# Performance work log

Measured on AMD Instinct MI355X. Metric: run time of the kernel, lower is better.

Reference implementation:

```python
import jax, jax.numpy as jnp
import numpy as np

IN_FEATURES = 512
OUT_FEATURES = 1024
BATCH = 1024
LAMBD = 0.2
TOL = 1e-4
MAX_ITERS = 100


def setup_inputs() -> dict:
    key = jax.random.key(0)
    kx, kw = jax.random.split(key)
    x = jax.random.normal(kx, (BATCH, IN_FEATURES), dtype=jnp.float32)
    # weight ~ randn(out, in), normalized over dim=0 (per-column) as in torch
    w = jax.random.normal(kw, (OUT_FEATURES, IN_FEATURES), dtype=jnp.float32)
    w = w / jnp.linalg.norm(w, axis=0)
    # M_inv = inverse(A^T A + I)^T with A = weight.T of shape (N, M)
    A = w.T  # (N, M)
    Mmat = A.T @ A + jnp.eye(OUT_FEATURES, dtype=jnp.float32)  # (M, M)
    M_inv = jnp.linalg.inv(Mmat).T
    return {"x": x, "weight": w, "M_inv": M_inv}


def _softshrink(x, lambd):
    return jnp.sign(x) * jnp.maximum(jnp.abs(x) - lambd, 0.0)


def _admm(A_dot_b, M_inv, lambd):
    # Fixed-length scan with per-sample freeze masks, equivalent to the
    # torch loop that removes converged rows from the active batch.
    B, M = A_dot_b.shape
    z = jnp.zeros((B, M), A_dot_b.dtype)
    solved0 = jnp.zeros((B,), dtype=bool)
    # carry: (v, u, v_prev, v_solution, solved)
    def step(carry, _):
        v, u, v_prev, v_sol, solved = carry
        b_eff = A_dot_b + v - u               # (B, M)
        xk = b_eff @ M_inv                    # (B, M)
        v_new = _softshrink(xk + u, lambd)
        u_new = u + xk - v_new
        dx_norm = jnp.linalg.norm(v_new - v_prev, axis=1)
        x_norm = jnp.linalg.norm(v_new, axis=1)
        conv = (dx_norm / x_norm) < TOL       # nan (0/0) compares False, as torch
        newly = conv & (~solved)
        v_sol = jnp.where(newly[:, None], v_new, v_sol)
        solved = solved | newly
        active = ~solved
        # frozen (solved) rows stop updating, mirroring removal from the batch
        v2 = jnp.where(active[:, None], v_new, v)
        u2 = jnp.where(active[:, None], u_new, u)
        return (v2, u2, v2, v_sol, solved), None

    carry0 = (z, z, z, z, solved0)
    (v, u, v_prev, v_sol, solved), _ = jax.lax.scan(step, carry0, None, length=MAX_ITERS)
    # torch returns v_solution (zeros for never-converged samples)
    return v_sol


def reference(x, weight, M_inv):
    input_shape = x.shape
    b = jax.lax.stop_gradient(x.reshape(x.shape[0], -1))  # x.detach().flatten(1)
    A_dot_b = b @ weight.T  # b @ A with A = weight.T -> (B, M)
    encoded = _admm(A_dot_b, M_inv, LAMBD)  # (B, M)
    decoded = encoded @ weight              # (B, N)
    return encoded, decoded.reshape(input_shape)
```

## Files before the change

### kernel.cpp

```cpp
#include <hip/hip_runtime.h>

typedef _Float16 half8 __attribute__((ext_vector_type(8)));
typedef _Float16 half4 __attribute__((ext_vector_type(4)));
typedef float floatx4 __attribute__((ext_vector_type(4)));
typedef float floatx16 __attribute__((ext_vector_type(16)));

static constexpr int BATCH = 1024;
static constexpr int NIN   = 512;
static constexpr int MOUT  = 1024;
static constexpr float LAMBD = 0.2f;
static constexpr float TOLF  = 1e-4f;
static constexpr int MAX_ITERS = 100;
static constexpr int MM = BATCH * MOUT;

__device__ __forceinline__ size_t swz(int idx, int k) {
    return ((((size_t)(idx >> 4) * 32 + (k >> 5)) * 64 +
             ((idx & 15) | (((k >> 3) & 3) << 4))) << 3) + (k & 7);
}

__device__ __forceinline__ size_t swz32(int idx, int k) {
    return ((((size_t)(idx >> 5) * 64 + (k >> 4)) * 64 +
             ((idx & 31) | (((k >> 3) & 1) << 5))) << 3) + (k & 7);
}

__device__ __forceinline__ float shrinkf(float t) {
    float a = fabsf(t) - LAMBD;
    return a > 0.f ? copysignf(a, t) : 0.f;
}

__device__ __forceinline__ void gbar32(int* cnt, int* gen, int seq) {
    __syncthreads();
    if (threadIdx.x == 0) {
        int old = atomicAdd(cnt, 1);
        if (old == seq * 32 - 1) {
            __hip_atomic_store(gen, seq, __ATOMIC_RELAXED,
                               __HIP_MEMORY_SCOPE_AGENT);
        } else {
            while (__hip_atomic_load(gen, __ATOMIC_RELAXED,
                                     __HIP_MEMORY_SCOPE_AGENT) < seq)
                __builtin_amdgcn_s_sleep(1);
        }
    }
    __syncthreads();
    asm volatile("buffer_inv sc0" ::: "memory");
}

__global__ __launch_bounds__(256) void zero_init(float* t, float* enc,
                                                 float* dec, float* ench_f,
                                                 float* encl_f, int* solved) {
    int i = blockIdx.x * 256 + threadIdx.x;
    if (i < MM) { t[i] = 0.f; enc[i] = 0.f; }
    if (i < MM / 2) { dec[i] = 0.f; ench_f[i] = 0.f; encl_f[i] = 0.f; }
    if (i < 4096) solved[i] = 0;
}

__global__ __launch_bounds__(256) void split_minv(const float* __restrict__ Minv,
                                                  _Float16* __restrict__ Th,
                                                  _Float16* __restrict__ Tl) {
    int g = blockIdx.x * 256 + threadIdx.x;
    int n = g & 1023, k0 = (g >> 10) << 3;
    half8 h, l;
    #pragma unroll
    for (int e = 0; e < 8; ++e) {
        float val = Minv[(size_t)(k0 + e) * MOUT + n];
        _Float16 hh = (_Float16)val;
        h[e] = hh;
        l[e] = (_Float16)(val - (float)hh);
    }
    size_t off = swz32(n, k0);
    *(half8*)&Th[off] = h;
    *(half8*)&Tl[off] = l;
}

__global__ __launch_bounds__(256) void split_w(const float* __restrict__ w,
                                               _Float16* __restrict__ wsh,
                                               _Float16* __restrict__ wsl) {
    int g = blockIdx.x * 256 + threadIdx.x;
    int n = g & 511, k0 = (g >> 9) << 3;
    half8 h, l;
    #pragma unroll
    for (int e = 0; e < 8; ++e) {
        float val = w[(size_t)(k0 + e) * NIN + n];
        _Float16 hh = (_Float16)val;
        h[e] = hh;
        l[e] = (_Float16)(val - (float)hh);
    }
    size_t off = swz(n, k0);
    *(half8*)&wsh[off] = h;
    *(half8*)&wsl[off] = l;
}

__global__ __launch_bounds__(256) void gemm_adb(const float* __restrict__ x,
                                                const float* __restrict__ w,
                                                float* __restrict__ adb,
                                                _Float16* __restrict__ bh,
                                                _Float16* __restrict__ bl) {
    __shared__ float As[16][68];
    __shared__ float Bs[16][68];
    const int tid = threadIdx.x;
    const int i0 = (blockIdx.x >> 4) * 64, j0 = (blockIdx.x & 15) * 64;
    const int tx = tid & 15, ty = tid >> 4;
    const int lr = tid >> 2, lk = (tid & 3) << 2;
    float acc[4][4] = {};
    for (int k0 = 0; k0 < NIN; k0 += 16) {
        float4 a4 = *(const float4*)&x[(i0 + lr) * NIN + k0 + lk];
        As[lk + 0][lr] = a4.x; As[lk + 1][lr] = a4.y;
        As[lk + 2][lr] = a4.z; As[lk + 3][lr] = a4.w;
        float4 b4 = *(const float4*)&w[(j0 + lr) * NIN + k0 + lk];
        Bs[lk + 0][lr] = b4.x; Bs[lk + 1][lr] = b4.y;
        Bs[lk + 2][lr] = b4.z; Bs[lk + 3][lr] = b4.w;
        __syncthreads();
        #pragma unroll
        for (int kk = 0; kk < 16; ++kk) {
            float4 a_ = *(const float4*)&As[kk][ty << 2];
            float4 b_ = *(const float4*)&Bs[kk][tx << 2];
            #pragma unroll
            for (int r = 0; r < 4; ++r) {
                float av = r == 0 ? a_.x : r == 1 ? a_.y : r == 2 ? a_.z : a_.w;
                acc[r][0] = fmaf(av, b_.x, acc[r][0]);
                acc[r][1] = fmaf(av, b_.y, acc[r][1]);
                acc[r][2] = fmaf(av, b_.z, acc[r][2]);
                acc[r][3] = fmaf(av, b_.w, acc[r][3]);
            }
        }
        __syncthreads();
    }
    const int k4 = j0 + (tx << 2);
    #pragma unroll
    for (int r = 0; r < 4; ++r) {
        const int row = i0 + (ty << 2) + r;
        *(float4*)&adb[(size_t)row * MOUT + k4] =
            make_float4(acc[r][0], acc[r][1], acc[r][2], acc[r][3]);
        half4 h, l;
        #pragma unroll
        for (int e = 0; e < 4; ++e) {
            _Float16 hh = (_Float16)acc[r][e];
            h[e] = hh;
            l[e] = (_Float16)(acc[r][e] - (float)hh);
        }
        size_t off = swz32(row, k4);
        *(half4*)&bh[off] = h;
        *(half4*)&bl[off] = l;
    }
}

__global__ __launch_bounds__(512, 2)
void admm_loop(const float* __restrict__ adb, float* __restrict__ part,
               _Float16* __restrict__ bh0, _Float16* __restrict__ bl0,
               _Float16* __restrict__ bh1, _Float16* __restrict__ bl1,
               const _Float16* __restrict__ Th, const _Float16* __restrict__ Tl,
               float* __restrict__ enc, _Float16* __restrict__ ench,
               _Float16* __restrict__ encl, int* __restrict__ solved,
               int* __restrict__ bar) {
    const int bid = blockIdx.x;
    const int tid = threadIdx.x, lane = tid & 63;
    const int w = tid >> 6;
    const int bt = w >> 1;
    const int kh = w & 1;
    const int mt = bid & 7, nt = bid >> 3;
    const int n0 = nt << 5, m0 = mt << 7;
    const int hn = lane >> 5;
    const int brow = m0 + (bt << 5) + (lane & 31);
    const int btile = (mt << 2) + bt;

    __shared__ _Float16 Bs[128 * 512];
    __shared__ float sc[4][64][24];
    __shared__ int s_exit;

    #pragma unroll
    for (int q = 0; q < 16; ++q) {
        const int chunk = (w << 4) + q;
        const int kc = chunk >> 1, hl = chunk & 1;
        const _Float16* src = (hl ? Tl : Th) +
            (((size_t)((nt << 6) + kc)) << 9) + ((size_t)lane << 3);
        __builtin_amdgcn_global_load_lds(
            (const __attribute__((address_space(1))) void*)src,
            (__attribute__((address_space(3))) void*)&Bs[(size_t)chunk << 9],
            16, 0, 0);
    }
    __syncthreads();

    int* gcnt = bar + (mt << 5);
    int* ggen = bar + (mt << 5) + 16;

    float treg[16] = {};
    float adbreg[16];
    #pragma unroll
    for (int r4 = 0; r4 < 4; ++r4) {
        const int nb = n0 + (r4 << 3) + (hn << 2);
        float4 a4 = *(const float4*)&adb[(size_t)brow * MOUT + nb];
        adbreg[(r4 << 2) + 0] = a4.x; adbreg[(r4 << 2) + 1] = a4.y;
        adbreg[(r4 << 2) + 2] = a4.z; adbreg[(r4 << 2) + 3] = a4.w;
    }
    bool sflag = false;

    for (int it = 0; it < MAX_ITERS; ++it) {
        const _Float16* rbh = (it & 1) ? bh1 : bh0;
        const _Float16* rbl = (it & 1) ? bl1 : bl0;
        _Float16* wbh = (it & 1) ? bh0 : bh1;
        _Float16* wbl = (it & 1) ? bl0 : bl1;

        floatx16 accA = {}, accB = {}, accC = {};
        const int kc0 = kh << 5;
        #pragma unroll 4
        for (int kc = kc0; kc < kc0 + 32; ++kc) {
            const size_t boff =
                (((size_t)(btile << 6) + kc) << 9) + ((size_t)lane << 3);
            const half8 bhf = *(const half8*)&rbh[boff];
            const half8 blf = *(const half8*)&rbl[boff];
            const half8 ah = *(const half8*)&Bs[((kc << 1) << 9) + (lane << 3)];
            const half8 al = *(const half8*)&Bs[(((kc << 1) | 1) << 9) + (lane << 3)];
            accA = __builtin_amdgcn_mfma_f32_32x32x16_f16(al, bhf, accA, 0, 0, 0);
            accB = __builtin_amdgcn_mfma_f32_32x32x16_f16(ah, blf, accB, 0, 0, 0);
            accC = __builtin_amdgcn_mfma_f32_32x32x16_f16(ah, bhf, accC, 0, 0, 0);
        }
        if (kh) {
            #pragma unroll
            for (int r4 = 0; r4 < 4; ++r4) {
                float4 v;
                v.x = (accA[(r4 << 2) + 0] + accB[(r4 << 2) + 0]) + accC[(r4 << 2) + 0];
                v.y = (accA[(r4 << 2) + 1] + accB[(r4 << 2) + 1]) + accC[(r4 << 2) + 1];
                v.z = (accA[(r4 << 2) + 2] + accB[(r4 << 2) + 2]) + accC[(r4 << 2) + 2];
                v.w = (accA[(r4 << 2) + 3] + accB[(r4 << 2) + 3]) + accC[(r4 << 2) + 3];
                *(float4*)&sc[bt][lane][r4 << 2] = v;
            }
        }
        __syncthreads();

        float dx2 = 0.f, x2 = 0.f;
        if (kh == 0 && !sflag) {
            #pragma unroll
            for (int r4 = 0; r4 < 4; ++r4) {
                float4 p1 = *(const float4*)&sc[bt][lane][r4 << 2];
                float pa[4] = {p1.x, p1.y, p1.z, p1.w};
                half4 h, l;
                #pragma unroll
                for (int e = 0; e < 4; ++e) {
                    const int r = (r4 << 2) + e;
                    float s0 = (accA[r] + accB[r]) + accC[r];
                    float xk = s0 + pa[e];
                    float t_ = treg[r];
                    float vprev = shrinkf(t_);
                    float uu = t_ - vprev;
                    float tn = xk + uu;
                    float vv = shrinkf(tn);
                    float un = tn - vv;
                    float d = vv - vprev;
                    dx2 += d * d;
                    x2 += vv * vv;
                    treg[r] = tn;
                    float nb_ = (adbreg[r] + vv) - un;
                    _Float16 hh = (_Float16)nb_;
                    h[e] = hh;
                    l[e] = (_Float16)(nb_ - (float)hh);
                }
                size_t off = swz32(brow, n0 + (r4 << 3) + (hn << 2));
                *(half4*)&wbh[off] = h;
                *(half4*)&wbl[off] = l;
            }
            dx2 += __shfl_xor(dx2, 32);
            x2  += __shfl_xor(x2, 32);
            if (hn == 0)
                *(float2*)&part[(((size_t)brow << 5) | nt) << 1] =
                    make_float2(dx2, x2);
        }
        gbar32(gcnt, ggen, 2 * it + 1);

        if (w < 4) {
            const int urow = m0 + (nt << 2) + w;
            if (!((volatile const int*)solved)[urow]) {
                float2 p = *(const float2*)
                    &part[(((size_t)urow << 5) | (lane & 31)) << 1];
                float rdx = p.x, rx = p.y;
                #pragma unroll
                for (int off = 16; off; off >>= 1) {
                    rdx += __shfl_xor(rdx, off);
                    rx  += __shfl_xor(rx, off);
                }
                if (rdx < TOLF * TOLF * rx) {
                    if (lane == 0) ((volatile int*)solved)[urow] = 1;
                }
            }
        }
        gbar32(gcnt, ggen, 2 * it + 2);

        sflag = ((volatile const int*)solved)[brow] != 0;
        if (tid == 0) s_exit = 0;
        __syncthreads();
        if (kh == 0 && !sflag && lane < 32) s_exit = 1;
        __syncthreads();
        if (s_exit == 0) break;
    }

    if (kh == 0 && sflag) {
        #pragma unroll
        for (int r4 = 0; r4 < 4; ++r4) {
            const int nb = n0 + (r4 << 3) + (hn << 2);
            float va[4]; half4 h, l;
            #pragma unroll
            for (int e = 0; e < 4; ++e) {
                float vv = shrinkf(treg[(r4 << 2) + e]);
                va[e] = vv;
                _Float16 hh = (_Float16)vv;
                h[e] = hh;
                l[e] = (_Float16)(vv - (float)hh);
            }
            *(float4*)&enc[(size_t)brow * MOUT + nb] =
                make_float4(va[0], va[1], va[2], va[3]);
            size_t off = swz(brow, nb);
            *(half4*)&ench[off] = h;
            *(half4*)&encl[off] = l;
        }
    }
}

__global__ __launch_bounds__(256, 2)
void mfma_dec(const _Float16* __restrict__ Ahg, const _Float16* __restrict__ Alg,
              const _Float16* __restrict__ Bhg, const _Float16* __restrict__ Blg,
              float* __restrict__ out) {
    constexpr int NSTR = NIN;
    constexpr int NT = NSTR / 128;
    const int bid = blockIdx.x;
    const int c = bid & 7, t = bid >> 3;
    const int mt = t / NT, nt = t % NT;
    const int tid = threadIdx.x, lane = tid & 63;

    __shared__ _Float16 Ash[64 * 512];

    const int wv = tid >> 6;
    const int wm = (tid >> 7) & 1, wn = (tid >> 6) & 1;
    const int kf0 = c << 2;

    #pragma unroll
    for (int i = 0; i < 16; ++i) {
        const int chunk = (wv << 4) + i;
        const int rt = chunk >> 3, kc = (chunk >> 1) & 3, hl = chunk & 1;
        const _Float16* src = (hl ? Alg : Ahg) +
            ((((size_t)((mt << 3) + rt) * 32 + kf0 + kc) << 9) + ((size_t)lane << 3));
        __builtin_amdgcn_global_load_lds(
            (const __attribute__((address_space(1))) void*)src,
            (__attribute__((address_space(3))) void*)&Ash[(size_t)chunk << 9],
            16, 0, 0);
    }
    __syncthreads();

    const int ct0 = nt * 8 + (wn << 2);
    const _Float16* pBh = Bhg + ((((size_t)ct0 * 32 + kf0) * 64 + lane) << 3);
    const _Float16* pBl = Blg + ((((size_t)ct0 * 32 + kf0) * 64 + lane) << 3);

    floatx4 acc[4][4] = {};
    #pragma unroll
    for (int s = 0; s < 4; ++s) {
        half8 bhf[4], blf[4];
        #pragma unroll
        for (int j = 0; j < 4; ++j) {
            bhf[j] = *(const half8*)(pBh + ((size_t)j << 14) + ((size_t)s << 9));
            blf[j] = *(const half8*)(pBl + ((size_t)j << 14) + ((size_t)s << 9));
        }
        half8 ah[4], al[4];
        #pragma unroll
        for (int i = 0; i < 4; ++i) {
            const int rt = (wm << 2) + i;
            ah[i] = *(const half8*)&Ash[((((rt << 2) + s) << 1) << 9) + (lane << 3)];
            al[i] = *(const half8*)&Ash[(((((rt << 2) + s) << 1) + 1) << 9) + (lane << 3)];
        }
        #pragma unroll
        for (int i = 0; i < 4; ++i)
            #pragma unroll
            for (int j = 0; j < 4; ++j) {
                acc[i][j] = __builtin_amdgcn_mfma_f32_16x16x32_f16(
                    ah[i], blf[j], acc[i][j], 0, 0, 0);
                acc[i][j] = __builtin_amdgcn_mfma_f32_16x16x32_f16(
                    al[i], bhf[j], acc[i][j], 0, 0, 0);
                acc[i][j] = __builtin_amdgcn_mfma_f32_16x16x32_f16(
                    ah[i], bhf[j], acc[i][j], 0, 0, 0);
            }
    }

    const int orow = (lane >> 4) << 2;
    #pragma unroll
    for (int i = 0; i < 4; ++i) {
        const int gr = (mt << 7) + (wm << 6) + (i << 4) + orow;
        #pragma unroll
        for (int j = 0; j < 4; ++j) {
            const int gc = nt * 128 + (wn << 6) + (j << 4) + (lane & 15);
            #pragma unroll
            for (int r = 0; r < 4; ++r)
                atomicAdd(&out[(size_t)(gr + r) * NSTR + gc], acc[i][j][r]);
        }
    }
}

extern "C" void kernel_launch(void* const* d_in, const int* in_sizes, int n_in,
                              void* d_out, int out_size, void* d_ws, size_t ws_size,
                              hipStream_t stream) {
    const float* x    = (const float*)d_in[0];
    const float* w    = (const float*)d_in[1];
    const float* Minv = (const float*)d_in[2];

    float* enc = (float*)d_out;
    float* dec = enc + MM;

    float* ws  = (float*)d_ws;
    float* adb = ws;
    _Float16* bh1 = (_Float16*)(ws + (size_t)MM);
    _Float16* bl1 = bh1 + (size_t)MM;
    float* part = ws + 2 * (size_t)MM;

    _Float16* bh0  = (_Float16*)(ws + 4 * (size_t)MM);
    _Float16* bl0  = bh0 + (size_t)MM;
    _Float16* Th   = bl0 + (size_t)MM;
    _Float16* Tl   = Th + (size_t)MM;
    _Float16* ench = Tl + (size_t)MM;
    _Float16* encl = ench + (size_t)MM;
    _Float16* wsh  = encl + (size_t)MM;
    _Float16* wsl  = wsh + (size_t)(NIN * MOUT);
    int* solved    = (int*)(wsl + (size_t)(NIN * MOUT));
    int* bar       = solved + 1088;

    zero_init<<<(MM + 255) / 256, 256, 0, stream>>>((float*)bh1, enc, dec,
                                                    (float*)ench, (float*)encl,
                                                    solved);
    split_minv<<<512, 256, 0, stream>>>(Minv, Th, Tl);
    split_w<<<256, 256, 0, stream>>>(w, wsh, wsl);
    gemm_adb<<<256, 256, 0, stream>>>(x, w, adb, bh0, bl0);

    void* cargs[] = {(void*)&adb, (void*)&part,
                     (void*)&bh0, (void*)&bl0, (void*)&bh1, (void*)&bl1,
                     (void*)&Th,  (void*)&Tl,
                     (void*)&enc, (void*)&ench, (void*)&encl, (void*)&solved,
                     (void*)&bar};
    hipLaunchCooperativeKernel(reinterpret_cast<void*>(admm_loop),
                               dim3(256), dim3(512), cargs, 0, stream);

    mfma_dec<<<256, 256, 0, stream>>>(ench, encl, wsh, wsl, dec);
}
```

Baseline: 1.289 ms.

## Fold convergence check into next iteration to halve grid barriers per ADMM step

Each block now computes per-row convergence itself from double-buffered partial norms, reading the previous iteration's partials during the next MFMA phase. This removes the second grid barrier and the global solved array, keeping the freeze flags in shared memory. The change also alters the shared scratch layout to avoid bank conflicts and relaxes launch bounds to one block per CU. It risks redundant reduction work across blocks and a slightly different exit timing, handled by a final check after the loop.

New measurement: 1.038 ms (median of 2 runs). 19.5% less time.

```diff
diff --git a/kernel.cpp b/kernel.cpp
--- a/kernel.cpp
+++ b/kernel.cpp
@@ -144,14 +144,13 @@
     }
 }
 
-__global__ __launch_bounds__(512, 2)
+__global__ __launch_bounds__(512, 1)
 void admm_loop(const float* __restrict__ adb, float* __restrict__ part,
                _Float16* __restrict__ bh0, _Float16* __restrict__ bl0,
                _Float16* __restrict__ bh1, _Float16* __restrict__ bl1,
                const _Float16* __restrict__ Th, const _Float16* __restrict__ Tl,
                float* __restrict__ enc, _Float16* __restrict__ ench,
-               _Float16* __restrict__ encl, int* __restrict__ solved,
-               int* __restrict__ bar) {
+               _Float16* __restrict__ encl, int* __restrict__ bar) {
     const int bid = blockIdx.x;
     const int tid = threadIdx.x, lane = tid & 63;
     const int w = tid >> 6;
@@ -164,8 +163,10 @@
     const int btile = (mt << 2) + bt;
 
     __shared__ _Float16 Bs[128 * 512];
-    __shared__ float sc[4][64][24];
-    __shared__ int s_exit;
+    __shared__ float4 sc4[4][4][64];
+    __shared__ unsigned char sfroz[128];
+
+    if (tid < 128) sfroz[tid] = 0;
 
     #pragma unroll
     for (int q = 0; q < 16; ++q) {
@@ -183,6 +184,10 @@
     int* gcnt = bar + (mt << 5);
     int* ggen = bar + (mt << 5) + 16;
 
+    const int drow_l = (w << 4) + (lane >> 2);
+    const int dq = (lane & 3) << 3;
+    const float* dbase0 = part + ((((size_t)(m0 + drow_l)) << 6) + (dq << 1));
+
     float treg[16] = {};
     float adbreg[16];
     #pragma unroll
@@ -192,13 +197,23 @@
         adbreg[(r4 << 2) + 0] = a4.x; adbreg[(r4 << 2) + 1] = a4.y;
         adbreg[(r4 << 2) + 2] = a4.z; adbreg[(r4 << 2) + 3] = a4.w;
     }
-    bool sflag = false;
-
-    for (int it = 0; it < MAX_ITERS; ++it) {
+
+    int it = 0;
+    for (; it < MAX_ITERS; ++it) {
         const _Float16* rbh = (it & 1) ? bh1 : bh0;
         const _Float16* rbl = (it & 1) ? bl1 : bl0;
         _Float16* wbh = (it & 1) ? bh0 : bh1;
         _Float16* wbl = (it & 1) ? bl0 : bl1;
+        const int pw = it & 1;
+
+        float4 dp0, dp1, dp2, dp3;
+        if (it) {
+            const float* pb = dbase0 + ((size_t)(pw ^ 1) << 16);
+            dp0 = *(const float4*)(pb + 0);
+            dp1 = *(const float4*)(pb + 4);
+            dp2 = *(const float4*)(pb + 8);
+            dp3 = *(const float4*)(pb + 12);
+        }
 
         floatx16 accA = {}, accB = {}, accC = {};
         const int kc0 = kh << 5;
@@ -222,16 +237,31 @@
                 v.y = (accA[(r4 << 2) + 1] + accB[(r4 << 2) + 1]) + accC[(r4 << 2) + 1];
                 v.z = (accA[(r4 << 2) + 2] + accB[(r4 << 2) + 2]) + accC[(r4 << 2) + 2];
                 v.w = (accA[(r4 << 2) + 3] + accB[(r4 << 2) + 3]) + accC[(r4 << 2) + 3];
-                *(float4*)&sc[bt][lane][r4 << 2] = v;
+                sc4[bt][r4][lane] = v;
             }
         }
+
+        if (it) {
+            float rdx = ((dp0.x + dp0.z) + (dp1.x + dp1.z)) +
+                        ((dp2.x + dp2.z) + (dp3.x + dp3.z));
+            float rx  = ((dp0.y + dp0.w) + (dp1.y + dp1.w)) +
+                        ((dp2.y + dp2.w) + (dp3.y + dp3.w));
+            rdx += __shfl_xor(rdx, 1); rdx += __shfl_xor(rdx, 2);
+            rx  += __shfl_xor(rx, 1);  rx  += __shfl_xor(rx, 2);
+            if (rdx < TOLF * TOLF * rx && (lane & 3) == 0)
+                sfroz[drow_l] = 1;
+        }
         __syncthreads();
 
-        float dx2 = 0.f, x2 = 0.f;
+        bool f0 = sfroz[lane] != 0, f1 = sfroz[64 + lane] != 0;
+        if ((__ballot(f0) & __ballot(f1)) == ~0ull) break;
+
+        const bool sflag = sfroz[(bt << 5) + (lane & 31)] != 0;
         if (kh == 0 && !sflag) {
+            float dx2 = 0.f, x2 = 0.f;
             #pragma unroll
             for (int r4 = 0; r4 < 4; ++r4) {
-                float4 p1 = *(const float4*)&sc[bt][lane][r4 << 2];
+                float4 p1 = sc4[bt][r4][lane];
                 float pa[4] = {p1.x, p1.y, p1.z, p1.w};
                 half4 h, l;
                 #pragma unroll
@@ -261,38 +291,31 @@
             dx2 += __shfl_xor(dx2, 32);
             x2  += __shfl_xor(x2, 32);
             if (hn == 0)
-                *(float2*)&part[(((size_t)brow << 5) | nt) << 1] =
+                *(float2*)&part[(((size_t)pw << 16) +
+                                 (((size_t)brow) << 6) + ((size_t)nt << 1))] =
                     make_float2(dx2, x2);
         }
-        gbar32(gcnt, ggen, 2 * it + 1);
-
-        if (w < 4) {
-            const int urow = m0 + (nt << 2) + w;
-            if (!((volatile const int*)solved)[urow]) {
-                float2 p = *(const float2*)
-                    &part[(((size_t)urow << 5) | (lane & 31)) << 1];
-                float rdx = p.x, rx = p.y;
-                #pragma unroll
-                for (int off = 16; off; off >>= 1) {
-                    rdx += __shfl_xor(rdx, off);
-                    rx  += __shfl_xor(rx, off);
-                }
-                if (rdx < TOLF * TOLF * rx) {
-                    if (lane == 0) ((volatile int*)solved)[urow] = 1;
-                }
-            }
-        }
-        gbar32(gcnt, ggen, 2 * it + 2);
-
-        sflag = ((volatile const int*)solved)[brow] != 0;
-        if (tid == 0) s_exit = 0;
+        gbar32(gcnt, ggen, it + 1);
+    }
+
+    if (it == MAX_ITERS) {
+        const float* pb = dbase0 + ((size_t)((MAX_ITERS - 1) & 1) << 16);
+        float4 dp0 = *(const float4*)(pb + 0);
+        float4 dp1 = *(const float4*)(pb + 4);
+        float4 dp2 = *(const float4*)(pb + 8);
+        float4 dp3 = *(const float4*)(pb + 12);
+        float rdx = ((dp0.x + dp0.z) + (dp1.x + dp1.z)) +
+                    ((dp2.x + dp2.z) + (dp3.x + dp3.z));
+        float rx  = ((dp0.y + dp0.w) + (dp1.y + dp1.w)) +
+                    ((dp2.y + dp2.w) + (dp3.y + dp3.w));
+        rdx += __shfl_xor(rdx, 1); rdx += __shfl_xor(rdx, 2);
+        rx  += __shfl_xor(rx, 1);  rx  += __shfl_xor(rx, 2);
+        if (rdx < TOLF * TOLF * rx && (lane & 3) == 0)
+            sfroz[drow_l] = 1;
         __syncthreads();
-        if (kh == 0 && !sflag && lane < 32) s_exit = 1;
-        __syncthreads();
-        if (s_exit == 0) break;
-    }
-
-    if (kh == 0 && sflag) {
+    }
+
+    if (kh == 0 && sfroz[(bt << 5) + (lane & 31)]) {
         #pragma unroll
         for (int r4 = 0; r4 < 4; ++r4) {
             const int nb = n0 + (r4 << 3) + (hn << 2);
@@ -428,8 +451,7 @@
     void* cargs[] = {(void*)&adb, (void*)&part,
                      (void*)&bh0, (void*)&bl0, (void*)&bh1, (void*)&bl1,
                      (void*)&Th,  (void*)&Tl,
-                     (void*)&enc, (void*)&ench, (void*)&encl, (void*)&solved,
-                     (void*)&bar};
+                     (void*)&enc, (void*)&ench, (void*)&encl, (void*)&bar};
     hipLaunchCooperativeKernel(reinterpret_cast<void*>(admm_loop),
                                dim3(256), dim3(512), cargs, 0, stream);
 
```
